# Performance work log

Hardware: AMD Instinct MI355X
Metric: run time of the kernel (lower is better)

## Reference

```python
import jax, jax.numpy as jnp
import numpy as np

LAYER_SIZE = 8192

def setup_inputs() -> dict:
    key = jax.random.key(0)
    kx, kw = jax.random.split(key)
    x = jax.random.normal(kx, (LAYER_SIZE,), dtype=jnp.float32)
    # ParameterList rows initialized with torch.rand -> uniform [0,1); stored as a
    # dense [n,n] matrix whose strict upper triangle is unused (masked in reference).
    W = jax.random.uniform(kw, (LAYER_SIZE, LAYER_SIZE), dtype=jnp.float32)
    return {"x": x, "W": W}

def reference(x, W):
    # y[i] = sum_{j<=i} W[i,j] * x[j] : lower-triangular matvec.
    L = jnp.tril(W)
    return L @ x
```

## Files before the change

kernel.cpp:

```cpp
#include <hip/hip_runtime.h>

#define LT_N 8192

__global__ __launch_bounds__(256, 4) void tril_matvec_kernel(
    const float* __restrict__ x,
    const float* __restrict__ W,
    float* __restrict__ y)
{
    __shared__ float xs[LT_N];

    {
        const float4* x4 = (const float4*)x;
        float4* xs4 = (float4*)xs;
        for (int i = threadIdx.x; i < LT_N / 4; i += 256) xs4[i] = x4[i];
    }
    __syncthreads();

    const int wave = threadIdx.x >> 6;
    const int lane = threadIdx.x & 63;
    const int r = LT_N - 1 - (int)(blockIdx.x * 4 + wave);
    const int len = r + 1;
    const int len4 = len & ~3;

    const float* Wr = W + (size_t)r * LT_N;

    float acc = 0.0f;
    for (int j = lane * 4; j < len4; j += 64 * 4) {
        float4 w  = *(const float4*)(Wr + j);
        float4 xv = *(const float4*)(xs + j);
        acc += w.x * xv.x + w.y * xv.y + w.z * xv.z + w.w * xv.w;
    }
    const int rem = len - len4;
    if (lane < rem) acc += Wr[len4 + lane] * xs[len4 + lane];

    #pragma unroll
    for (int off = 32; off > 0; off >>= 1)
        acc += __shfl_down(acc, off, 64);

    if (lane == 0) y[r] = acc;
}

extern "C" void kernel_launch(void* const* d_in, const int* in_sizes, int n_in,
                              void* d_out, int out_size, void* d_ws, size_t ws_size,
                              hipStream_t stream)
{
    const float* x = (const float*)d_in[0];
    const float* W = (const float*)d_in[1];
    float* y = (float*)d_out;

    dim3 grid(LT_N / 4);
    dim3 block(256);
    tril_matvec_kernel<<<grid, block, 0, stream>>>(x, W, y);
}
```

Before: 323.1 us.

## Pair short and long triangular rows per wave for balanced work

Each wave now computes two rows, r and N-1-r, so every wave handles about N+1 elements and the triangular load is balanced. The grid shrinks to 1024 blocks, which also halves the shared-memory x staging per row. The long-row tail loop is unrolled by two with separate accumulators to keep more loads in flight. The cost is more registers and fewer blocks in total, which lowers the parallelism available to hide latency.

```diff
diff --git a/kernel.cpp b/kernel.cpp
--- a/kernel.cpp
+++ b/kernel.cpp
@@ -12,32 +12,67 @@
     {
         const float4* x4 = (const float4*)x;
         float4* xs4 = (float4*)xs;
-        for (int i = threadIdx.x; i < LT_N / 4; i += 256) xs4[i] = x4[i];
+        #pragma unroll
+        for (int i = 0; i < 8; ++i)
+            xs4[threadIdx.x + i * 256] = x4[threadIdx.x + i * 256];
     }
     __syncthreads();
 
     const int wave = threadIdx.x >> 6;
     const int lane = threadIdx.x & 63;
-    const int r = LT_N - 1 - (int)(blockIdx.x * 4 + wave);
-    const int len = r + 1;
-    const int len4 = len & ~3;
+    const int w = blockIdx.x * 4 + wave;
+    const int rA = w;
+    const int rB = LT_N - 1 - w;
 
-    const float* Wr = W + (size_t)r * LT_N;
+    const float* WrA = W + (size_t)rA * LT_N;
+    const float* WrB = W + (size_t)rB * LT_N;
+    const int lenA  = rA + 1;
+    const int lenB  = rB + 1;
+    const int lenA4 = lenA & ~3;
+    const int lenB4 = lenB & ~3;
 
-    float acc = 0.0f;
-    for (int j = lane * 4; j < len4; j += 64 * 4) {
-        float4 w  = *(const float4*)(Wr + j);
+    float accA = 0.f, accB0 = 0.f, accB1 = 0.f;
+
+    int j = lane * 4;
+
+    for (; j < lenA4; j += 256) {
+        float4 a  = *(const float4*)(WrA + j);
+        float4 b  = *(const float4*)(WrB + j);
         float4 xv = *(const float4*)(xs + j);
-        acc += w.x * xv.x + w.y * xv.y + w.z * xv.z + w.w * xv.w;
+        accA  += a.x * xv.x + a.y * xv.y + a.z * xv.z + a.w * xv.w;
+        accB0 += b.x * xv.x + b.y * xv.y + b.z * xv.z + b.w * xv.w;
     }
-    const int rem = len - len4;
-    if (lane < rem) acc += Wr[len4 + lane] * xs[len4 + lane];
+    for (; j + 256 < lenB4; j += 512) {
+        float4 b0 = *(const float4*)(WrB + j);
+        float4 b1 = *(const float4*)(WrB + j + 256);
+        float4 x0 = *(const float4*)(xs + j);
+        float4 x1 = *(const float4*)(xs + j + 256);
+        accB0 += b0.x * x0.x + b0.y * x0.y + b0.z * x0.z + b0.w * x0.w;
+        accB1 += b1.x * x1.x + b1.y * x1.y + b1.z * x1.z + b1.w * x1.w;
+    }
+    for (; j < lenB4; j += 256) {
+        float4 b0 = *(const float4*)(WrB + j);
+        float4 x0 = *(const float4*)(xs + j);
+        accB0 += b0.x * x0.x + b0.y * x0.y + b0.z * x0.z + b0.w * x0.w;
+    }
+
+    const int remA = lenA - lenA4;
+    if (lane < remA) accA  += WrA[lenA4 + lane] * xs[lenA4 + lane];
+    const int remB = lenB - lenB4;
+    if (lane < remB) accB0 += WrB[lenB4 + lane] * xs[lenB4 + lane];
+
+    float accB = accB0 + accB1;
 
     #pragma unroll
-    for (int off = 32; off > 0; off >>= 1)
-        acc += __shfl_down(acc, off, 64);
+    for (int off = 32; off > 0; off >>= 1) {
+        accA += __shfl_down(accA, off, 64);
+        accB += __shfl_down(accB, off, 64);
+    }
 
-    if (lane == 0) y[r] = acc;
+    if (lane == 0) {
+        y[rA] = accA;
+        y[rB] = accB;
+    }
 }
 
 extern "C" void kernel_launch(void* const* d_in, const int* in_sizes, int n_in,
@@ -48,7 +83,7 @@
     const float* W = (const float*)d_in[1];
     float* y = (float*)d_out;
 
-    dim3 grid(LT_N / 4);
+    dim3 grid(1024);
     dim3 block(256);
     tril_matvec_kernel<<<grid, block, 0, stream>>>(x, W, y);
 }
```

Measured after the change: 323.2 us. Within noise of the previous version (+0.0%).

## Assign one row per block split across waves, drop shared-memory x staging

Applied to the files above, without the earlier changes.

Each block now handles one row, with its four waves each covering a 2048-column chunk. Partial sums are combined through shared memory. The 32KB shared-memory copy of x is removed and x is read directly from global memory, where it should stay cached in L2. Full chunks use an unrolled path that issues 8 float4 loads per operand up front to raise memory-level parallelism. The trade-off is four times as many blocks, an extra block-wide sync, and idle waves on short rows.

```diff
diff --git a/kernel.cpp b/kernel.cpp
--- a/kernel.cpp
+++ b/kernel.cpp
@@ -1,43 +1,60 @@
 #include <hip/hip_runtime.h>
 
 #define LT_N 8192
+#define CHUNK 2048
 
 __global__ __launch_bounds__(256, 4) void tril_matvec_kernel(
     const float* __restrict__ x,
     const float* __restrict__ W,
     float* __restrict__ y)
 {
-    __shared__ float xs[LT_N];
-
-    {
-        const float4* x4 = (const float4*)x;
-        float4* xs4 = (float4*)xs;
-        for (int i = threadIdx.x; i < LT_N / 4; i += 256) xs4[i] = x4[i];
-    }
-    __syncthreads();
+    __shared__ float partial[4];
 
     const int wave = threadIdx.x >> 6;
     const int lane = threadIdx.x & 63;
-    const int r = LT_N - 1 - (int)(blockIdx.x * 4 + wave);
+    const int r = LT_N - 1 - (int)blockIdx.x;
     const int len = r + 1;
-    const int len4 = len & ~3;
-
     const float* Wr = W + (size_t)r * LT_N;
 
+    const int beg = wave * CHUNK;
+    const int end = min(beg + CHUNK, len);
+
     float acc = 0.0f;
-    for (int j = lane * 4; j < len4; j += 64 * 4) {
-        float4 w  = *(const float4*)(Wr + j);
-        float4 xv = *(const float4*)(xs + j);
-        acc += w.x * xv.x + w.y * xv.y + w.z * xv.z + w.w * xv.w;
+    if (beg < len) {
+        const int n = end - beg;
+        if (n == CHUNK) {
+            const float* Wb = Wr + beg + lane * 4;
+            const float* xb = x  + beg + lane * 4;
+            float4 wv[8], xv[8];
+            #pragma unroll
+            for (int i = 0; i < 8; ++i) wv[i] = *(const float4*)(Wb + i * 256);
+            #pragma unroll
+            for (int i = 0; i < 8; ++i) xv[i] = *(const float4*)(xb + i * 256);
+            #pragma unroll
+            for (int i = 0; i < 8; ++i)
+                acc += wv[i].x * xv[i].x + wv[i].y * xv[i].y
+                     + wv[i].z * xv[i].z + wv[i].w * xv[i].w;
+        } else {
+            const int n4 = n & ~3;
+            for (int j = lane * 4; j < n4; j += 256) {
+                float4 wv = *(const float4*)(Wr + beg + j);
+                float4 xv = *(const float4*)(x  + beg + j);
+                acc += wv.x * xv.x + wv.y * xv.y + wv.z * xv.z + wv.w * xv.w;
+            }
+            const int rem = n - n4;
+            if (lane < rem)
+                acc += Wr[beg + n4 + lane] * x[beg + n4 + lane];
+        }
     }
-    const int rem = len - len4;
-    if (lane < rem) acc += Wr[len4 + lane] * xs[len4 + lane];
 
     #pragma unroll
     for (int off = 32; off > 0; off >>= 1)
         acc += __shfl_down(acc, off, 64);
 
-    if (lane == 0) y[r] = acc;
+    if (lane == 0) partial[wave] = acc;
+    __syncthreads();
+    if (threadIdx.x == 0)
+        y[r] = (partial[0] + partial[1]) + (partial[2] + partial[3]);
 }
 
 extern "C" void kernel_launch(void* const* d_in, const int* in_sizes, int n_in,
@@ -48,7 +65,7 @@
     const float* W = (const float*)d_in[1];
     float* y = (float*)d_out;
 
-    dim3 grid(LT_N / 4);
+    dim3 grid(LT_N);
     dim3 block(256);
     tril_matvec_kernel<<<grid, block, 0, stream>>>(x, W, y);
 }
```

After: 323.9 us (median of 2 runs). No clear change (+0.3%).
